# Performance work log

Measured on AMD Instinct MI355X. Metric: run time of the kernel, lower is better.

Reference implementation:

```python
import jax, jax.numpy as jnp
import numpy as np

K = 4
TEMPERATURE = 30.0


def setup_inputs() -> dict:
    key = jax.random.key(0)
    ks = jax.random.split(key, 6)
    B, C, H, W_sp = 32, 128, 56, 56
    Cout, kh, kw = 128, 3, 3
    Cred = max(C // 4, 1)
    x = jax.random.normal(ks[0], (B, C, H, W_sp), dtype=jnp.float32)
    # K parallel conv kernels + biases (fan-in scaled init)
    fan = C * kh * kw
    W = jax.random.normal(ks[1], (K, Cout, C, kh, kw), dtype=jnp.float32) / np.sqrt(fan)
    b = jax.random.normal(ks[2], (K, Cout), dtype=jnp.float32) * 0.01
    # attention branch: 1x1 convs == dense on pooled features
    aw1 = jax.random.normal(ks[3], (Cred, C), dtype=jnp.float32) / np.sqrt(C)
    aw2 = jax.random.normal(ks[4], (K, Cred), dtype=jnp.float32) / np.sqrt(Cred)
    return {"x": x, "W": W, "b": b, "aw1": aw1, "aw2": aw2}


def reference(x, W, b, aw1, aw2):
    # attention: global avg pool -> 1x1 conv (dense) -> relu -> 1x1 conv -> softmax(logits/T)
    pooled = jnp.mean(x, axis=(2, 3))                       # [B, C]
    h1 = jax.nn.relu(jnp.einsum('bc,rc->br', pooled, aw1))  # [B, Cred]
    logits = jnp.einsum('br,kr->bk', h1, aw2)               # [B, K]
    attn = jax.nn.softmax(logits / TEMPERATURE, axis=1)     # [B, K]

    pad = 1
    out = None
    for i in range(K):  # fixed small K, structurally distinct kernels
        yi = jax.lax.conv_general_dilated(
            x, W[i], window_strides=(1, 1), padding=[(pad, pad), (pad, pad)],
            dimension_numbers=('NCHW', 'OIHW', 'NCHW'))
        yi = yi + b[i][None, :, None, None]
        yi = yi * attn[:, i][:, None, None, None]
        out = yi if out is None else out + yi
    return out
```

## Files before the change

kernel.cpp:

```cpp
#include <hip/hip_runtime.h>
#include <hip/hip_bf16.h>
#include <stdint.h>

typedef __bf16 bf16x8 __attribute__((ext_vector_type(8)));
typedef float  f32x4  __attribute__((ext_vector_type(4)));
typedef unsigned short u16x8 __attribute__((ext_vector_type(8)));

#define NB 32
#define NC 128
#define NH 56
#define NW 56
#define NK 4
#define NCO 128
#define NCR 32
#define NHW 3136
#define TEMPER 30.0f

#define WS_ATTN   0u
#define WS_BC     4096u
#define WS_ROWSUM 65536u
#define WS_WC     1048576u
#define WS_XT     10485760u

__global__ void xt_kernel(const float* __restrict__ x, __hip_bfloat16* __restrict__ xt,
                          float* __restrict__ rowsum) {
  __shared__ float lds[58 * 133];
  int xcd = blockIdx.x & 7;
  int j   = blockIdx.x >> 3;
  int b   = xcd * 4 + j / 58;
  int hp  = j % 58;
  int blk = b * 58 + hp;
  int h = hp - 1;
  bool hin = (h >= 0) && (h < NH);
  int tid = threadIdx.x;
  if (hin) {
    const float* xrow = x + ((size_t)b * NC) * NHW + (size_t)h * NW;
    for (int i = tid; i < 128 * 14; i += 256) {
      int c = i / 14;
      int w4 = (i - c * 14) * 4;
      float4 v = *(const float4*)(xrow + (size_t)c * NHW + w4);
      int base = (w4 + 1) * 133 + c;
      lds[base]         = v.x;
      lds[base + 133]   = v.y;
      lds[base + 2*133] = v.z;
      lds[base + 3*133] = v.w;
    }
  }
  __syncthreads();
  __hip_bfloat16* orow = xt + (size_t)blk * (58 * 128);
  for (int i = tid; i < 58 * 16; i += 256) {
    int wp = i >> 4;
    int cg = (i & 15) << 3;
    u16x8 o;
    if (!hin || wp == 0 || wp == 57) {
      o = (u16x8)0;
    } else {
      const float* src = lds + wp * 133 + cg;
      #pragma unroll
      for (int jx = 0; jx < 8; ++jx) {
        union { __hip_bfloat16 b; unsigned short u; } cv;
        cv.b = __float2bfloat16(src[jx]);
        o[jx] = cv.u;
      }
    }
    *(u16x8*)(orow + wp * 128 + cg) = o;
  }
  if (hin && tid < 128) {
    float s = 0.f;
    #pragma unroll 8
    for (int wp = 1; wp <= 56; ++wp) s += lds[wp * 133 + tid];
    rowsum[(size_t)blk * 128 + tid] = s;
  }
}

__global__ void attn_kernel(const float* __restrict__ rowsum, const float* __restrict__ aw1,
                            const float* __restrict__ aw2, const float* __restrict__ bias,
                            float* __restrict__ attn, float* __restrict__ bc_out) {
  int b = blockIdx.x;
  __shared__ float sp[NC], h1[NCR], at[NK];
  int t = threadIdx.x;
  if (t < NC) {
    float s = 0.f;
    for (int hp = 1; hp <= 56; ++hp) s += rowsum[((size_t)b * 58 + hp) * 128 + t];
    sp[t] = s * (1.0f / (float)NHW);
  }
  __syncthreads();
  if (t < NCR) {
    float s = 0.f;
    for (int c = 0; c < NC; ++c) s += aw1[t*NC + c] * sp[c];
    h1[t] = s > 0.f ? s : 0.f;
  }
  __syncthreads();
  if (t == 0) {
    float lg[NK], mx = -1e30f;
    for (int k = 0; k < NK; ++k) {
      float s = 0.f;
      for (int r = 0; r < NCR; ++r) s += aw2[k*NCR + r] * h1[r];
      lg[k] = s * (1.0f/TEMPER);
      mx = fmaxf(mx, lg[k]);
    }
    float den = 0.f, e[NK];
    for (int k = 0; k < NK; ++k) { e[k] = expf(lg[k]-mx); den += e[k]; }
    float inv = 1.0f/den;
    for (int k = 0; k < NK; ++k) { at[k] = e[k]*inv; attn[b*NK+k] = at[k]; }
  }
  __syncthreads();
  if (t < NCO) {
    float s = 0.f;
    for (int k = 0; k < NK; ++k) s += at[k] * bias[k*NCO + t];
    bc_out[b*NCO + t] = s;
  }
}

__global__ void combine_kernel(const float* __restrict__ W, const float* __restrict__ attn,
                               __hip_bfloat16* __restrict__ wc) {
  int gid = blockIdx.x;
  int bg  = gid >> 6;
  int tcell = (gid & 63) * 256 + threadIdx.x;
  int co = tcell >> 7, ci = tcell & 127;
  float w[4][9];
  const float* wp = W + ((size_t)co * 128 + ci) * 9;
  #pragma unroll
  for (int k = 0; k < 4; ++k)
    #pragma unroll
    for (int j = 0; j < 9; ++j)
      w[k][j] = wp[(size_t)k * 147456 + j];
  for (int b = bg * 8; b < bg * 8 + 8; ++b) {
    float a0 = attn[b*4+0], a1 = attn[b*4+1], a2 = attn[b*4+2], a3 = attn[b*4+3];
    #pragma unroll
    for (int j = 0; j < 9; ++j) {
      float v = a0*w[0][j] + a1*w[1][j] + a2*w[2][j] + a3*w[3][j];
      wc[(((size_t)b*9 + j) * 128 + co) * 128 + ci] = __float2bfloat16(v);
    }
  }
}

#define RS 2368
#define CS 40
#define BBUF (10*RS)
#define ABUF (9*128*32)

#define GLOAD16(src, dst) \
  __builtin_amdgcn_global_load_lds( \
    (const __attribute__((address_space(1))) unsigned int*)(src), \
    (__attribute__((address_space(3))) unsigned int*)(dst), 16, 0, 0)

__global__ __launch_bounds__(512, 2) void conv_kernel(
    const unsigned short* __restrict__ xt,
    const unsigned short* __restrict__ wc,
    const float* __restrict__ bc,
    float* __restrict__ out) {
  __shared__ __align__(16) unsigned short lds_a[ABUF];
  __shared__ __align__(16) unsigned short lds_b[BBUF];
  const int tid  = threadIdx.x;
  const int lane = tid & 63;
  const int wv   = tid >> 6;
  const int wm   = wv >> 2;
  const int wn   = wv & 3;
  const int bid  = blockIdx.x;
  const int xcd  = bid & 7;
  const int jj   = bid >> 3;
  const int b    = xcd*4 + jj/7;
  const int r0   = (jj % 7) * 8;
  const int li   = lane & 15;
  const int kg   = lane >> 4;

  int srcB[6];
  #pragma unroll
  for (int i = 0; i < 6; ++i) {
    int q = i*512 + tid;
    int r = q / 296;
    int sl = q - r*296;
    int col = sl / 5;
    int part = sl - col*5;
    srcB[i] = (q < 2960 && col < 58 && part < 4)
              ? ((r0 + r)*58 + col)*128 + part*8 : -1;
  }
  int srcA[9];
  #pragma unroll
  for (int i = 0; i < 9; ++i) {
    int c = i*512 + tid;
    int khw  = c >> 9;
    int co   = (c & 511) >> 2;
    int part = c & 3;
    srcA[i] = (khw*128 + co)*128 + part*8;
  }

  int xoff[7];
  #pragma unroll
  for (int f = 0; f < 7; ++f) {
    int pos = wn*112 + f*16 + li;
    int rB = pos / 56;
    int cB = pos - rB*56;
    xoff[f] = rB*RS + cB*CS + kg*8;
  }
  const int aRead = (wm*64 + li)*32 + kg*8;

  const f32x4 vzero = {0.f, 0.f, 0.f, 0.f};
  f32x4 acc[4][7];
  #pragma unroll
  for (int mo = 0; mo < 4; ++mo)
    #pragma unroll
    for (int f = 0; f < 7; ++f) acc[mo][f] = vzero;

  const unsigned short* xtg = xt + (size_t)b*(58*58*128);
  const unsigned short* wcg = wc + (size_t)b*(9*128*128);

  #define LOADFRAG(AF, BF, khw) do { \
    const int kh_ = (khw)/3, kw_ = (khw)-kh_*3; \
    _Pragma("unroll") \
    for (int mo = 0; mo < 4; ++mo) \
      AF[mo] = *(const bf16x8*)(lds_a + (khw)*4096 + aRead + mo*512); \
    const int koff_ = kh_*RS + kw_*CS; \
    _Pragma("unroll") \
    for (int f = 0; f < 7; ++f) \
      BF[f] = *(const bf16x8*)(lds_b + xoff[f] + koff_); \
  } while (0)

  #define DOMFMA(AF, BF) do { \
    _Pragma("unroll") \
    for (int mo = 0; mo < 4; ++mo) \
      _Pragma("unroll") \
      for (int f = 0; f < 7; ++f) \
        acc[mo][f] = __builtin_amdgcn_mfma_f32_16x16x32_bf16(AF[mo], BF[f], acc[mo][f], 0, 0, 0); \
  } while (0)

  for (int cc = 0; cc < 4; ++cc) {
    if (cc > 0) __syncthreads();
    #pragma unroll
    for (int i = 0; i < 9; ++i)
      GLOAD16(wcg + srcA[i] + cc*32, lds_a + (i*512 + wv*64)*8);
    #pragma unroll
    for (int i = 0; i < 6; ++i)
      if (srcB[i] >= 0)
        GLOAD16(xtg + srcB[i] + cc*32, lds_b + (i*512 + wv*64)*8);
    __syncthreads();

    bf16x8 afE[4], bfE[7], afO[4], bfO[7];
    LOADFRAG(afE, bfE, 0);
    LOADFRAG(afO, bfO, 1);
    DOMFMA(afE, bfE);
    LOADFRAG(afE, bfE, 2);
    DOMFMA(afO, bfO);
    LOADFRAG(afO, bfO, 3);
    DOMFMA(afE, bfE);
    LOADFRAG(afE, bfE, 4);
    DOMFMA(afO, bfO);
    LOADFRAG(afO, bfO, 5);
    DOMFMA(afE, bfE);
    LOADFRAG(afE, bfE, 6);
    DOMFMA(afO, bfO);
    LOADFRAG(afO, bfO, 7);
    DOMFMA(afE, bfE);
    LOADFRAG(afE, bfE, 8);
    DOMFMA(afO, bfO);
    DOMFMA(afE, bfE);
  }

  float* ob = out + (size_t)b*NCO*NHW;
  #pragma unroll
  for (int mo = 0; mo < 4; ++mo) {
    #pragma unroll
    for (int rg = 0; rg < 4; ++rg) {
      const int co = wm*64 + mo*16 + kg*4 + rg;
      const float bv = bc[b*NCO + co];
      float* orow = ob + (size_t)co*NHW;
      #pragma unroll
      for (int f = 0; f < 7; ++f) {
        int pos = wn*112 + f*16 + li;
        int rB = pos / 56;
        int cB = pos - rB*56;
        orow[(r0 + rB)*56 + cB] = acc[mo][f][rg] + bv;
      }
    }
  }
}

extern "C" void kernel_launch(void* const* d_in, const int* in_sizes, int n_in,
                              void* d_out, int out_size, void* d_ws, size_t ws_size,
                              hipStream_t stream) {
  const float* x   = (const float*)d_in[0];
  const float* W   = (const float*)d_in[1];
  const float* bia = (const float*)d_in[2];
  const float* aw1 = (const float*)d_in[3];
  const float* aw2 = (const float*)d_in[4];
  float* out = (float*)d_out;
  char* ws = (char*)d_ws;
  float* attn   = (float*)(ws + WS_ATTN);
  float* bcm    = (float*)(ws + WS_BC);
  float* rowsum = (float*)(ws + WS_ROWSUM);
  __hip_bfloat16* wc = (__hip_bfloat16*)(ws + WS_WC);
  __hip_bfloat16* xt = (__hip_bfloat16*)(ws + WS_XT);

  xt_kernel<<<NB*58, 256, 0, stream>>>(x, xt, rowsum);
  attn_kernel<<<NB, 128, 0, stream>>>(rowsum, aw1, aw2, bia, attn, bcm);
  combine_kernel<<<256, 256, 0, stream>>>(W, attn, wc);
  conv_kernel<<<224, 512, 0, stream>>>((const unsigned short*)xt,
                                       (const unsigned short*)wc, bcm, out);
}
```

Before: 66.85 us.

## Double-buffer LDS staging per kernel row to overlap global loads with MFMA

Replaces the load-all-then-compute loop over channel chunks with a 12-step software pipeline. Weights are staged one kernel row (3 taps) at a time and input tiles one channel chunk at a time, each into double-buffered LDS, with explicit vmcnt waits and raw barriers so the next stage's global-to-LDS loads overlap the current MFMAs. It also raises wave priority around the MFMA blocks and clamps out-of-range source indices instead of skipping those loads. The cost is a larger LDS footprint per block, which may hurt the 2-blocks-per-CU occupancy, and fragile hand-counted waitcnt values.

```diff
diff --git a/kernel.cpp b/kernel.cpp
--- a/kernel.cpp
+++ b/kernel.cpp
@@ -137,8 +137,8 @@
 
 #define RS 2368
 #define CS 40
-#define BBUF (10*RS)
-#define ABUF (9*128*32)
+#define BBUF (3072*8)
+#define ABUF (1536*8)
 
 #define GLOAD16(src, dst) \
   __builtin_amdgcn_global_load_lds( \
@@ -150,8 +150,8 @@
     const unsigned short* __restrict__ wc,
     const float* __restrict__ bc,
     float* __restrict__ out) {
-  __shared__ __align__(16) unsigned short lds_a[ABUF];
-  __shared__ __align__(16) unsigned short lds_b[BBUF];
+  __shared__ __align__(16) unsigned short lds_a[2*ABUF];
+  __shared__ __align__(16) unsigned short lds_b[2*BBUF];
   const int tid  = threadIdx.x;
   const int lane = tid & 63;
   const int wv   = tid >> 6;
@@ -173,17 +173,19 @@
     int sl = q - r*296;
     int col = sl / 5;
     int part = sl - col*5;
-    srcB[i] = (q < 2960 && col < 58 && part < 4)
-              ? ((r0 + r)*58 + col)*128 + part*8 : -1;
-  }
-  int srcA[9];
-  #pragma unroll
-  for (int i = 0; i < 9; ++i) {
+    int rc = r  > 9  ? 9  : r;
+    int cc_ = col > 57 ? 57 : col;
+    int pc = part > 3 ? 3 : part;
+    srcB[i] = ((r0 + rc)*58 + cc_)*128 + pc*8;
+  }
+  int srcA[3];
+  #pragma unroll
+  for (int i = 0; i < 3; ++i) {
     int c = i*512 + tid;
-    int khw  = c >> 9;
+    int khwL = c >> 9;
     int co   = (c & 511) >> 2;
     int part = c & 3;
-    srcA[i] = (khw*128 + co)*128 + part*8;
+    srcA[i] = (khwL*128 + co)*128 + part*8;
   }
 
   int xoff[7];
@@ -206,56 +208,73 @@
   const unsigned short* xtg = xt + (size_t)b*(58*58*128);
   const unsigned short* wcg = wc + (size_t)b*(9*128*128);
 
-  #define LOADFRAG(AF, BF, khw) do { \
-    const int kh_ = (khw)/3, kw_ = (khw)-kh_*3; \
+  #define STAGE_B(bufidx, ccn) do { \
+    unsigned short* dbase = lds_b + (bufidx)*BBUF + wv*512; \
+    _Pragma("unroll") \
+    for (int i = 0; i < 6; ++i) \
+      GLOAD16(xtg + srcB[i] + (ccn)*32, dbase + i*4096); \
+  } while (0)
+
+  #define STAGE_A(bufidx, ccn, khn) do { \
+    unsigned short* dbase = lds_a + (bufidx)*ABUF + wv*512; \
+    _Pragma("unroll") \
+    for (int i = 0; i < 3; ++i) \
+      GLOAD16(wcg + (khn)*49152 + srcA[i] + (ccn)*32, dbase + i*4096); \
+  } while (0)
+
+  #define LOADFRAG(AF, BF, pa, pb, kwl, kh) do { \
     _Pragma("unroll") \
     for (int mo = 0; mo < 4; ++mo) \
-      AF[mo] = *(const bf16x8*)(lds_a + (khw)*4096 + aRead + mo*512); \
-    const int koff_ = kh_*RS + kw_*CS; \
+      AF[mo] = *(const bf16x8*)((pa) + (kwl)*4096 + aRead + mo*512); \
     _Pragma("unroll") \
     for (int f = 0; f < 7; ++f) \
-      BF[f] = *(const bf16x8*)(lds_b + xoff[f] + koff_); \
+      BF[f] = *(const bf16x8*)((pb) + xoff[f] + (kh)*RS + (kwl)*CS); \
   } while (0)
 
   #define DOMFMA(AF, BF) do { \
+    __builtin_amdgcn_s_setprio(1); \
     _Pragma("unroll") \
     for (int mo = 0; mo < 4; ++mo) \
       _Pragma("unroll") \
       for (int f = 0; f < 7; ++f) \
         acc[mo][f] = __builtin_amdgcn_mfma_f32_16x16x32_bf16(AF[mo], BF[f], acc[mo][f], 0, 0, 0); \
-  } while (0)
-
-  for (int cc = 0; cc < 4; ++cc) {
-    if (cc > 0) __syncthreads();
-    #pragma unroll
-    for (int i = 0; i < 9; ++i)
-      GLOAD16(wcg + srcA[i] + cc*32, lds_a + (i*512 + wv*64)*8);
-    #pragma unroll
-    for (int i = 0; i < 6; ++i)
-      if (srcB[i] >= 0)
-        GLOAD16(xtg + srcB[i] + cc*32, lds_b + (i*512 + wv*64)*8);
-    __syncthreads();
-
-    bf16x8 afE[4], bfE[7], afO[4], bfO[7];
-    LOADFRAG(afE, bfE, 0);
-    LOADFRAG(afO, bfO, 1);
-    DOMFMA(afE, bfE);
-    LOADFRAG(afE, bfE, 2);
-    DOMFMA(afO, bfO);
-    LOADFRAG(afO, bfO, 3);
-    DOMFMA(afE, bfE);
-    LOADFRAG(afE, bfE, 4);
-    DOMFMA(afO, bfO);
-    LOADFRAG(afO, bfO, 5);
-    DOMFMA(afE, bfE);
-    LOADFRAG(afE, bfE, 6);
-    DOMFMA(afO, bfO);
-    LOADFRAG(afO, bfO, 7);
-    DOMFMA(afE, bfE);
-    LOADFRAG(afE, bfE, 8);
-    DOMFMA(afO, bfO);
-    DOMFMA(afE, bfE);
-  }
+    __builtin_amdgcn_s_setprio(0); \
+  } while (0)
+
+  #define STEP(s, cc, kh, VM) do { \
+    if ((kh) == 0 && (cc) < 3) STAGE_B(((cc)+1)&1, (cc)+1); \
+    if ((s) < 11) STAGE_A(((s)+1)&1, ((s)+1)/3, ((s)+1)%3); \
+    asm volatile("s_waitcnt vmcnt(" #VM ")" ::: "memory"); \
+    __builtin_amdgcn_s_barrier(); \
+    { \
+      const unsigned short* pa = lds_a + ((s)&1)*ABUF; \
+      const unsigned short* pb = lds_b + ((cc)&1)*BBUF; \
+      bf16x8 afE[4], bfE[7], afO[4], bfO[7]; \
+      LOADFRAG(afE, bfE, pa, pb, 0, kh); \
+      LOADFRAG(afO, bfO, pa, pb, 1, kh); \
+      DOMFMA(afE, bfE); \
+      LOADFRAG(afE, bfE, pa, pb, 2, kh); \
+      DOMFMA(afO, bfO); \
+      DOMFMA(afE, bfE); \
+    } \
+    __builtin_amdgcn_s_barrier(); \
+  } while (0)
+
+  STAGE_B(0, 0);
+  STAGE_A(0, 0, 0);
+
+  STEP(0, 0, 0, 9);
+  STEP(1, 0, 1, 3);
+  STEP(2, 0, 2, 3);
+  STEP(3, 1, 0, 9);
+  STEP(4, 1, 1, 3);
+  STEP(5, 1, 2, 3);
+  STEP(6, 2, 0, 9);
+  STEP(7, 2, 1, 3);
+  STEP(8, 2, 2, 3);
+  STEP(9, 3, 0, 3);
+  STEP(10, 3, 1, 3);
+  STEP(11, 3, 2, 0);
 
   float* ob = out + (size_t)b*NCO*NHW;
   #pragma unroll
```

Result: no change. 67.93 us (+1.6%).
